# Optimization experiments

Measured on AMD Instinct MI355X. Metric: run time of the kernel, lower is better.

## Reference

```python
import jax, jax.numpy as jnp
import numpy as np

# E2M1 FP4 code table: code = sign(1b) | magnitude(3b)
FP4_VALS = jnp.array([0.0, 0.5, 1.0, 1.5, 2.0, 3.0, 4.0, 6.0,
                      -0.0, -0.5, -1.0, -1.5, -2.0, -3.0, -4.0, -6.0], dtype=jnp.float32)
ALPHA = 1.702
LIMIT = 7.0
BLOCK = 32


def dequant_mxfp4(qw, scales):
    """qw: [N, K//2] byte values (two 4-bit codes, low nibble first);
    scales: [N, K//32] E8M0 exponents. Returns fp32 [N, K]."""
    lo = qw & 0xF
    hi = (qw >> 4) & 0xF
    codes = jnp.stack([lo, hi], axis=-1).reshape(qw.shape[0], -1)  # [N, K]
    w = FP4_VALS[codes]
    s = jnp.exp2((scales - 127).astype(jnp.float32))               # [N, K//32]
    N, K = w.shape
    w = w.reshape(N, K // BLOCK, BLOCK) * s[..., None]
    return w.reshape(N, K)


def setup_inputs() -> dict:
    key = jax.random.key(0)
    ks = jax.random.split(key, 9)
    T, H, I, E, TOPK = 1024, 2880, 2880, 8, 2
    return {
        "hidden_states": jax.random.normal(ks[0], (T, H), dtype=jnp.float32),
        "routing_weights": jax.random.uniform(ks[1], (T, TOPK), dtype=jnp.float32),
        "gate_up_proj_bias": jax.random.normal(ks[2], (E, 2 * I), dtype=jnp.float32),
        "down_proj_bias": jax.random.normal(ks[3], (E, H), dtype=jnp.float32),
        "router_indices": jax.random.randint(ks[4], (T, TOPK), 0, E, dtype=jnp.int32),
        "gate_up_qweight": jax.random.randint(ks[5], (E, 2 * I, H // 2), 0, 256, dtype=jnp.int32),
        "gate_up_scales": jax.random.randint(ks[6], (E, 2 * I, H // BLOCK), 118, 130, dtype=jnp.int32),
        "down_qweight": jax.random.randint(ks[7], (E, H, I // 2), 0, 256, dtype=jnp.int32),
        "down_scales": jax.random.randint(ks[8], (E, H, I // BLOCK), 118, 130, dtype=jnp.int32),
    }


def reference(hidden_states, routing_weights, gate_up_proj_bias, down_proj_bias,
              router_indices, gate_up_qweight, gate_up_scales, down_qweight, down_scales):
    E = gate_up_qweight.shape[0]
    out = jnp.zeros_like(hidden_states)
    for e in range(E):  # small fixed expert count
        # combined routing weight per token for expert e (0 if not routed);
        # equals the index_add over all top_k hits in the original loop
        w_e = jnp.sum(jnp.where(router_indices == e, routing_weights, 0.0), axis=-1)  # [T]
        wg = dequant_mxfp4(gate_up_qweight[e], gate_up_scales[e])  # [2I, H]
        gate_up = hidden_states @ wg.T + gate_up_proj_bias[e]      # [T, 2I]
        gate = jnp.minimum(gate_up[..., 0::2], LIMIT)
        up = jnp.clip(gate_up[..., 1::2], -LIMIT, LIMIT)
        glu = gate * jax.nn.sigmoid(gate * ALPHA)
        gated = (up + 1.0) * glu                                   # [T, I]
        wd = dequant_mxfp4(down_qweight[e], down_scales[e])        # [H, I]
        o = gated @ wd.T + down_proj_bias[e]                       # [T, H]
        out = out + o * w_e[:, None]
    return out
```

## Files before the change

kernel.cpp:

```cpp
#include <hip/hip_runtime.h>
#include <hip/hip_bf16.h>

typedef unsigned int uint;
typedef unsigned short ushort;
typedef __bf16 bf16x8 __attribute__((ext_vector_type(8)));
typedef float f32x4 __attribute__((ext_vector_type(4)));
typedef unsigned short u16x2 __attribute__((ext_vector_type(2)));

#define T_TOK 1024
#define HDIM 2880
#define IDIM 2880
#define NEXP 8
#define GU 5760
#define QK1 1440
#define SG1 90
#define QK2 1440
#define SG2 90
#define MAXR 2048
#define NK 45

#define BM 384
#define BGU 192
#define BNH 64

#define LDA 72

#define LISTS_OFF 256
#define HB_OFF (1u << 17)
#define GATED_OFF_PRE 6029312u
#define GATED_OFF_RAW (1u << 17)
#define WS_NEED (GATED_OFF_PRE + (size_t)MAXR * IDIM * 2)


static __device__ __forceinline__ uint pkadd16(uint a, uint b) {
  u16x2 x = __builtin_bit_cast(u16x2, a);
  u16x2 y = __builtin_bit_cast(u16x2, b);
  u16x2 r = x + y;
  return __builtin_bit_cast(uint, r);
}

static __device__ __forceinline__ void decode8(uint P, uint sAdd2, uint out[4]) {
  uint L  = P & 0x0F0F0F0Fu;
  uint Hh = (P >> 4) & 0x0F0F0F0Fu;
  uint Lm = L & 0x07070707u,  Hm = Hh & 0x07070707u;
  uint Lsg = (L & 0x08080808u) << 4, Hsg = (Hh & 0x08080808u) << 4;
  uint hiL = __builtin_amdgcn_perm(0x40404040u, 0x3F3F3F00u, Lm) | Lsg;
  uint hiH = __builtin_amdgcn_perm(0x40404040u, 0x3F3F3F00u, Hm) | Hsg;
  uint loL = __builtin_amdgcn_perm(0xC0804000u, 0xC0800000u, Lm);
  uint loH = __builtin_amdgcn_perm(0xC0804000u, 0xC0800000u, Hm);
  uint mL  = __builtin_amdgcn_perm(0xFFFFFFFFu, 0xFFFFFF00u, Lm);
  uint mH  = __builtin_amdgcn_perm(0xFFFFFFFFu, 0xFFFFFF00u, Hm);
  uint pL01 = __builtin_amdgcn_perm(hiL, loL, 0x05010400u);
  uint pL23 = __builtin_amdgcn_perm(hiL, loL, 0x07030602u);
  uint pH01 = __builtin_amdgcn_perm(hiH, loH, 0x05010400u);
  uint pH23 = __builtin_amdgcn_perm(hiH, loH, 0x07030602u);
  uint aL01 = pkadd16(pL01, sAdd2 & __builtin_amdgcn_perm(mL, mL, 0x01010000u));
  uint aL23 = pkadd16(pL23, sAdd2 & __builtin_amdgcn_perm(mL, mL, 0x03030202u));
  uint aH01 = pkadd16(pH01, sAdd2 & __builtin_amdgcn_perm(mH, mH, 0x01010000u));
  uint aH23 = pkadd16(pH23, sAdd2 & __builtin_amdgcn_perm(mH, mH, 0x03030202u));
  out[0] = __builtin_amdgcn_perm(aH01, aL01, 0x05040100u);
  out[1] = __builtin_amdgcn_perm(aH01, aL01, 0x07060302u);
  out[2] = __builtin_amdgcn_perm(aH23, aL23, 0x05040100u);
  out[3] = __builtin_amdgcn_perm(aH23, aL23, 0x07060302u);
}

static __device__ __forceinline__ uint packbf2(float a, float b) {
  ushort ua = __builtin_bit_cast(ushort, __float2bfloat16(a));
  ushort ub = __builtin_bit_cast(ushort, __float2bfloat16(b));
  return (uint)ua | ((uint)ub << 16);
}


__global__ void build_lists_kernel(const int* __restrict__ ridx,
                                   int* __restrict__ counts,
                                   int* __restrict__ lists) {
  int r = blockIdx.x * 256 + threadIdx.x;
  if (r >= MAXR) return;
  int e = ridx[r];
  int pos = atomicAdd(&counts[e], 1);
  lists[e * MAXR + pos] = r;
}


__global__ void cvt_kernel(const float* __restrict__ in, ushort* __restrict__ out) {
  int i = (blockIdx.x * 256 + threadIdx.x) * 8;
  float4 a = *(const float4*)(in + i);
  float4 b = *(const float4*)(in + i + 4);
  uint4 o;
  o.x = packbf2(a.x, a.y); o.y = packbf2(a.z, a.w);
  o.z = packbf2(b.x, b.y); o.w = packbf2(b.z, b.w);
  *(uint4*)(out + i) = o;
}


template <bool PRE>
__global__ __launch_bounds__(512, 2)
void gemm1_kernel(const float* __restrict__ hiddenF,
                  const ushort* __restrict__ hiddenB,
                  const int* __restrict__ guq,
                  const int* __restrict__ gus,
                  const float* __restrict__ gub,
                  const int* __restrict__ counts,
                  const int* __restrict__ lists,
                  ushort* __restrict__ gated) {
  const int e = blockIdx.z;
  const int cnt = counts[e];
  const int mt = blockIdx.y;
  if (mt * BM >= cnt) return;
  const int gu0 = blockIdx.x * BGU;
  const int tid = threadIdx.x;

  extern __shared__ char smem[];
  ushort* lA = (ushort*)smem;
  ushort* lB = lA + BM * LDA;
  int* rowid = (int*)(lB + BGU * LDA);

  for (int i = tid; i < BM; i += 512) {
    int rl = mt * BM + i;
    rowid[i] = (rl < cnt) ? lists[e * MAXR + rl] : -1;
  }
  __syncthreads();

  const int srow = tid >> 3;
  const int soff = tid & 7;

  uint avalid = 0;
  const ushort* aB[6];
  const float*  aF[6];
  #pragma unroll
  for (int j = 0; j < 6; ++j) {
    int r = rowid[srow + 64 * j];
    if (r >= 0) avalid |= (1u << j);
    int tok = (r >= 0) ? (r >> 1) : 0;
    if (PRE) aB[j] = hiddenB + (size_t)tok * HDIM + soff * 8;
    else     aF[j] = hiddenF + (size_t)tok * HDIM + soff * 8;
  }
  const size_t jrow0 = (size_t)e * GU + gu0 + srow;
  const int* bq0 = guq + jrow0 * QK1 + soff * 4;
  const int* bs0 = gus + jrow0 * SG1 + (soff >> 2);

  f32x4 acc[6][6];
  #pragma unroll
  for (int m = 0; m < 6; ++m)
    #pragma unroll
    for (int n = 0; n < 6; ++n) acc[m][n] = (f32x4)0.f;

  const int ln = tid & 63;
  const int ln15 = ln & 15, kq = ln >> 4;
  const int wv = tid >> 6, wm = wv & 3, wn = wv >> 2;

  uint4 aP[6];
  int4  bP[3];
  int   sP[3];

  auto load_step = [&](int k0) {
    #pragma unroll
    for (int j = 0; j < 6; ++j) {
      if (avalid & (1u << j)) {
        if (PRE) {
          aP[j] = *(const uint4*)(aB[j] + k0);
        } else {
          float4 f0 = *(const float4*)(aF[j] + k0);
          float4 f1 = *(const float4*)(aF[j] + k0 + 4);
          aP[j].x = packbf2(f0.x, f0.y); aP[j].y = packbf2(f0.z, f0.w);
          aP[j].z = packbf2(f1.x, f1.y); aP[j].w = packbf2(f1.z, f1.w);
        }
      } else {
        aP[j].x = aP[j].y = aP[j].z = aP[j].w = 0u;
      }
    }
    #pragma unroll
    for (int j = 0; j < 3; ++j) {
      bP[j] = *(const int4*)(bq0 + (size_t)j * 64 * QK1 + (k0 >> 1));
      sP[j] = *(bs0 + (size_t)j * 64 * SG1 + (k0 >> 5));
    }
  };

  load_step(0);

  for (int ks = 0; ks < NK; ++ks) {
    #pragma unroll
    for (int j = 0; j < 6; ++j)
      *(uint4*)&lA[(srow + 64 * j) * LDA + soff * 8] = aP[j];
    #pragma unroll
    for (int j = 0; j < 3; ++j) {
      uint P = (uint)bP[j].x | ((uint)bP[j].y << 8) |
               ((uint)bP[j].z << 16) | ((uint)bP[j].w << 24);
      uint sOff = ((uint)(sP[j] - 127) << 7) & 0xFFFFu;
      uint sAdd2 = sOff | (sOff << 16);
      uint o[4];
      decode8(P, sAdd2, o);
      uint4 w; w.x = o[0]; w.y = o[1]; w.z = o[2]; w.w = o[3];
      *(uint4*)&lB[(srow + 64 * j) * LDA + soff * 8] = w;
    }
    __syncthreads();
    if (ks + 1 < NK) load_step((ks + 1) * 64);
    #pragma unroll
    for (int kf = 0; kf < 2; ++kf) {
      const int ko = kf * 32 + kq * 8;
      bf16x8 bfr[6];
      #pragma unroll
      for (int n = 0; n < 6; ++n)
        bfr[n] = *(const bf16x8*)&lB[(wn * 96 + n * 16 + ln15) * LDA + ko];
      #pragma unroll
      for (int m = 0; m < 6; ++m) {
        bf16x8 af = *(const bf16x8*)&lA[(wm * 96 + m * 16 + ln15) * LDA + ko];
        #pragma unroll
        for (int n = 0; n < 6; ++n)
          acc[m][n] = __builtin_amdgcn_mfma_f32_16x16x32_bf16(af, bfr[n], acc[m][n], 0, 0, 0);
      }
    }
    __syncthreads();
  }

  float bias[6];
  #pragma unroll
  for (int n = 0; n < 6; ++n)
    bias[n] = gub[(size_t)e * GU + gu0 + wn * 96 + n * 16 + ln15];
  #pragma unroll
  for (int m = 0; m < 6; ++m) {
    #pragma unroll
    for (int rg = 0; rg < 4; ++rg) {
      int rl = wm * 96 + m * 16 + kq * 4 + rg;
      int r = rowid[rl];
      #pragma unroll
      for (int n = 0; n < 6; ++n) {
        float x = acc[m][n][rg] + bias[n];
        float y = __shfl_xor(x, 1);
        if (r >= 0 && !(ln & 1)) {
          float g = fminf(x, 7.f);
          float u = fminf(fmaxf(y, -7.f), 7.f);
          float glu = g / (1.f + __expf(-1.702f * g));
          float val = (u + 1.f) * glu;
          int gucol = gu0 + wn * 96 + n * 16 + ln15;
          gated[(size_t)r * IDIM + (gucol >> 1)] =
              __builtin_bit_cast(ushort, __float2bfloat16(val));
        }
      }
    }
  }
}


__global__ __launch_bounds__(512, 2)
void gemm2_kernel(const ushort* __restrict__ gated,
                  const int* __restrict__ dq,
                  const int* __restrict__ dsc,
                  const float* __restrict__ dpb,
                  const float* __restrict__ routing,
                  const int* __restrict__ counts,
                  const int* __restrict__ lists,
                  float* __restrict__ outp) {
  const int e = blockIdx.z;
  const int cnt = counts[e];
  const int mt = blockIdx.y;
  if (mt * BM >= cnt) return;
  const int h0 = blockIdx.x * BNH;
  const int tid = threadIdx.x;

  extern __shared__ char smem[];
  ushort* lA = (ushort*)smem;
  ushort* lB = lA + BM * LDA;
  int* rowid = (int*)(lB + BNH * LDA);

  for (int i = tid; i < BM; i += 512) {
    int rl = mt * BM + i;
    rowid[i] = (rl < cnt) ? lists[e * MAXR + rl] : -1;
  }
  __syncthreads();

  const int srow = tid >> 3;
  const int soff = tid & 7;

  uint avalid = 0;
  const ushort* aB[6];
  #pragma unroll
  for (int j = 0; j < 6; ++j) {
    int r = rowid[srow + 64 * j];
    if (r >= 0) avalid |= (1u << j);
    int rr = (r >= 0) ? r : 0;
    aB[j] = gated + (size_t)rr * IDIM + soff * 8;
  }
  const size_t hrow = (size_t)e * HDIM + h0 + srow;
  const int* bq0 = dq + hrow * QK2 + soff * 4;
  const int* bs0 = dsc + hrow * SG2 + (soff >> 2);

  f32x4 acc[6][2];
  #pragma unroll
  for (int m = 0; m < 6; ++m) {
    acc[m][0] = (f32x4)0.f;
    acc[m][1] = (f32x4)0.f;
  }

  const int ln = tid & 63;
  const int ln15 = ln & 15, kq = ln >> 4;
  const int wv = tid >> 6, wm = wv & 3, wn = wv >> 2;

  uint4 aP[6];
  int4  bP;
  int   sP;

  auto load_step = [&](int k0) {
    #pragma unroll
    for (int j = 0; j < 6; ++j) {
      if (avalid & (1u << j)) aP[j] = *(const uint4*)(aB[j] + k0);
      else { aP[j].x = aP[j].y = aP[j].z = aP[j].w = 0u; }
    }
    bP = *(const int4*)(bq0 + (k0 >> 1));
    sP = *(bs0 + (k0 >> 5));
  };

  load_step(0);

  for (int ks = 0; ks < NK; ++ks) {
    #pragma unroll
    for (int j = 0; j < 6; ++j)
      *(uint4*)&lA[(srow + 64 * j) * LDA + soff * 8] = aP[j];
    {
      uint P = (uint)bP.x | ((uint)bP.y << 8) | ((uint)bP.z << 16) | ((uint)bP.w << 24);
      uint sOff = ((uint)(sP - 127) << 7) & 0xFFFFu;
      uint sAdd2 = sOff | (sOff << 16);
      uint o[4];
      decode8(P, sAdd2, o);
      uint4 w; w.x = o[0]; w.y = o[1]; w.z = o[2]; w.w = o[3];
      *(uint4*)&lB[srow * LDA + soff * 8] = w;
    }
    __syncthreads();
    if (ks + 1 < NK) load_step((ks + 1) * 64);
    #pragma unroll
    for (int kf = 0; kf < 2; ++kf) {
      const int ko = kf * 32 + kq * 8;
      bf16x8 bfr[2];
      #pragma unroll
      for (int n = 0; n < 2; ++n)
        bfr[n] = *(const bf16x8*)&lB[(wn * 32 + n * 16 + ln15) * LDA + ko];
      #pragma unroll
      for (int m = 0; m < 6; ++m) {
        bf16x8 af = *(const bf16x8*)&lA[(wm * 96 + m * 16 + ln15) * LDA + ko];
        #pragma unroll
        for (int n = 0; n < 2; ++n)
          acc[m][n] = __builtin_amdgcn_mfma_f32_16x16x32_bf16(af, bfr[n], acc[m][n], 0, 0, 0);
      }
    }
    __syncthreads();
  }

  float bias[2];
  #pragma unroll
  for (int n = 0; n < 2; ++n)
    bias[n] = dpb[(size_t)e * HDIM + h0 + wn * 32 + n * 16 + ln15];
  #pragma unroll
  for (int m = 0; m < 6; ++m) {
    #pragma unroll
    for (int rg = 0; rg < 4; ++rg) {
      int rl = wm * 96 + m * 16 + kq * 4 + rg;
      int r = rowid[rl];
      if (r < 0) continue;
      float wgt = routing[r];
      #pragma unroll
      for (int n = 0; n < 2; ++n) {
        int hcol = h0 + wn * 32 + n * 16 + ln15;
        atomicAdd(outp + (size_t)(r >> 1) * HDIM + hcol,
                  wgt * (acc[m][n][rg] + bias[n]));
      }
    }
  }
}


extern "C" void kernel_launch(void* const* d_in, const int* in_sizes, int n_in,
                              void* d_out, int out_size, void* d_ws, size_t ws_size,
                              hipStream_t stream) {
  const float* hidden  = (const float*)d_in[0];
  const float* routing = (const float*)d_in[1];
  const float* gub     = (const float*)d_in[2];
  const float* dpb     = (const float*)d_in[3];
  const int*   ridx    = (const int*)d_in[4];
  const int*   guq     = (const int*)d_in[5];
  const int*   gus     = (const int*)d_in[6];
  const int*   dq      = (const int*)d_in[7];
  const int*   dsc     = (const int*)d_in[8];
  float* outp = (float*)d_out;

  char* ws = (char*)d_ws;
  int* counts = (int*)ws;
  int* lists  = (int*)(ws + LISTS_OFF);
  const bool pre = (ws_size >= WS_NEED);
  ushort* hb    = (ushort*)(ws + HB_OFF);
  ushort* gated = (ushort*)(ws + (pre ? GATED_OFF_PRE : GATED_OFF_RAW));

  const int LDS1 = (BM * LDA + BGU * LDA) * 2 + BM * 4;
  const int LDS2 = (BM * LDA + BNH * LDA) * 2 + BM * 4;
  if (pre)
    hipFuncSetAttribute((const void*)gemm1_kernel<true>,
                        hipFuncAttributeMaxDynamicSharedMemorySize, LDS1);
  else
    hipFuncSetAttribute((const void*)gemm1_kernel<false>,
                        hipFuncAttributeMaxDynamicSharedMemorySize, LDS1);
  hipFuncSetAttribute((const void*)gemm2_kernel,
                      hipFuncAttributeMaxDynamicSharedMemorySize, LDS2);

  hipMemsetAsync(counts, 0, 256, stream);
  hipMemsetAsync(d_out, 0, (size_t)out_size * sizeof(float), stream);

  build_lists_kernel<<<MAXR / 256, 256, 0, stream>>>(ridx, counts, lists);
  if (pre)
    cvt_kernel<<<(T_TOK * HDIM / 8) / 256, 256, 0, stream>>>(hidden, hb);

  dim3 grid1(GU / BGU, (MAXR + BM - 1) / BM, NEXP);
  if (pre)
    gemm1_kernel<true><<<grid1, 512, LDS1, stream>>>(hidden, hb, guq, gus, gub,
                                                     counts, lists, gated);
  else
    gemm1_kernel<false><<<grid1, 512, LDS1, stream>>>(hidden, hb, guq, gus, gub,
                                                      counts, lists, gated);

  dim3 grid2(HDIM / BNH, (MAXR + BM - 1) / BM, NEXP);
  gemm2_kernel<<<grid2, 512, LDS2, stream>>>(gated, dq, dsc, dpb, routing,
                                             counts, lists, outp);
}
```

Baseline: 262.6 us.

## Retile expert GEMMs with async global-to-LDS loads and XOR-swizzled shared memory

Both expert GEMMs are restructured into 256-thread blocks with smaller N tiles (64 for gate/up, 32 for down) and a 320-row M tile, with experts interleaved in the x grid dimension. Activation tiles are now loaded straight into LDS with global_load_lds, using a zeroed dummy row for padding, in place of register staging. The padded LDS layout is replaced by an XOR swizzle, and s_setprio is raised around the MFMA section. This is meant to raise occupancy and cut register-staging and bank-conflict costs. In exchange it drops the previous register prefetch of the next step and decodes the weights more often because the N tiles are smaller.

```diff
diff --git a/kernel.cpp b/kernel.cpp
--- a/kernel.cpp
+++ b/kernel.cpp
@@ -18,19 +18,16 @@
 #define SG2 90
 #define MAXR 2048
 #define NK 45
-
-#define BM 384
-#define BGU 192
-#define BNH 64
-
-#define LDA 72
-
-#define LISTS_OFF 256
-#define HB_OFF (1u << 17)
+#define BM 320
+
+#define ZROW_OFF 65536u
+#define HB_OFF 131072u
 #define GATED_OFF_PRE 6029312u
-#define GATED_OFF_RAW (1u << 17)
 #define WS_NEED (GATED_OFF_PRE + (size_t)MAXR * IDIM * 2)
 
+static __device__ __forceinline__ int ls(int row, int c) {
+  return (row << 6) + (((c ^ row) & 7) << 3);
+}
 
 static __device__ __forceinline__ uint pkadd16(uint a, uint b) {
   u16x2 x = __builtin_bit_cast(u16x2, a);
@@ -94,137 +91,145 @@
 
 
 template <bool PRE>
-__global__ __launch_bounds__(512, 2)
-void gemm1_kernel(const float* __restrict__ hiddenF,
-                  const ushort* __restrict__ hiddenB,
+__global__ __launch_bounds__(256, 3)
+void gemm1_kernel(const char* __restrict__ wsb,
+                  const float* __restrict__ hiddenF,
                   const int* __restrict__ guq,
                   const int* __restrict__ gus,
                   const float* __restrict__ gub,
                   const int* __restrict__ counts,
                   const int* __restrict__ lists,
                   ushort* __restrict__ gated) {
-  const int e = blockIdx.z;
+  const int e  = blockIdx.x & 7;
+  const int xt = blockIdx.x >> 3;
   const int cnt = counts[e];
   const int mt = blockIdx.y;
   if (mt * BM >= cnt) return;
-  const int gu0 = blockIdx.x * BGU;
+  const int gu0 = xt * 64;
   const int tid = threadIdx.x;
 
-  extern __shared__ char smem[];
-  ushort* lA = (ushort*)smem;
-  ushort* lB = lA + BM * LDA;
-  int* rowid = (int*)(lB + BGU * LDA);
-
-  for (int i = tid; i < BM; i += 512) {
+  __shared__ ushort lA[BM * 64];
+  __shared__ ushort lB[64 * 64];
+  __shared__ int rowid[BM];
+
+  for (int i = tid; i < BM; i += 256) {
     int rl = mt * BM + i;
     rowid[i] = (rl < cnt) ? lists[e * MAXR + rl] : -1;
   }
   __syncthreads();
 
-  const int srow = tid >> 3;
-  const int soff = tid & 7;
-
+  const int ln = tid & 63, wv = tid >> 6;
+  const int ln15 = ln & 15, kq = ln >> 4;
+
+  uint aoff[10];
   uint avalid = 0;
-  const ushort* aB[6];
-  const float*  aF[6];
-  #pragma unroll
-  for (int j = 0; j < 6; ++j) {
-    int r = rowid[srow + 64 * j];
-    if (r >= 0) avalid |= (1u << j);
-    int tok = (r >= 0) ? (r >> 1) : 0;
-    if (PRE) aB[j] = hiddenB + (size_t)tok * HDIM + soff * 8;
-    else     aF[j] = hiddenF + (size_t)tok * HDIM + soff * 8;
-  }
-  const size_t jrow0 = (size_t)e * GU + gu0 + srow;
-  const int* bq0 = guq + jrow0 * QK1 + soff * 4;
-  const int* bs0 = gus + jrow0 * SG1 + (soff >> 2);
-
-  f32x4 acc[6][6];
-  #pragma unroll
-  for (int m = 0; m < 6; ++m)
-    #pragma unroll
-    for (int n = 0; n < 6; ++n) acc[m][n] = (f32x4)0.f;
-
-  const int ln = tid & 63;
-  const int ln15 = ln & 15, kq = ln >> 4;
-  const int wv = tid >> 6, wm = wv & 3, wn = wv >> 2;
-
-  uint4 aP[6];
-  int4  bP[3];
-  int   sP[3];
-
-  auto load_step = [&](int k0) {
-    #pragma unroll
-    for (int j = 0; j < 6; ++j) {
-      if (avalid & (1u << j)) {
-        if (PRE) {
-          aP[j] = *(const uint4*)(aB[j] + k0);
-        } else {
-          float4 f0 = *(const float4*)(aF[j] + k0);
-          float4 f1 = *(const float4*)(aF[j] + k0 + 4);
-          aP[j].x = packbf2(f0.x, f0.y); aP[j].y = packbf2(f0.z, f0.w);
-          aP[j].z = packbf2(f1.x, f1.y); aP[j].w = packbf2(f1.z, f1.w);
-        }
-      } else {
-        aP[j].x = aP[j].y = aP[j].z = aP[j].w = 0u;
-      }
-    }
-    #pragma unroll
-    for (int j = 0; j < 3; ++j) {
-      bP[j] = *(const int4*)(bq0 + (size_t)j * 64 * QK1 + (k0 >> 1));
-      sP[j] = *(bs0 + (size_t)j * 64 * SG1 + (k0 >> 5));
-    }
-  };
-
-  load_step(0);
+  if (PRE) {
+    #pragma unroll
+    for (int j = 0; j < 10; ++j) {
+      int slot = wv * 640 + j * 64 + ln;
+      int row  = slot >> 3;
+      int corig = (slot ^ row) & 7;
+      int r = rowid[row];
+      aoff[j] = (r >= 0) ? (HB_OFF + (uint)(r >> 1) * (HDIM * 2) + corig * 16)
+                         : (ZROW_OFF + corig * 16);
+    }
+  } else {
+    #pragma unroll
+    for (int j = 0; j < 10; ++j) {
+      int row = (tid >> 3) + 32 * j;
+      int r = rowid[row];
+      if (r >= 0) avalid |= 1u << j;
+      uint tok = (r >= 0) ? (uint)(r >> 1) : 0u;
+      aoff[j] = tok * (HDIM * 4) + (uint)(tid & 7) * 32;
+    }
+  }
+
+  const int brow = tid >> 2, c2 = tid & 3;
+  const uint grow = (uint)(e * GU + gu0 + brow);
+  const uint boff0 = grow * (QK1 * 4) + (uint)c2 * 32;
+  const uint soff0 = grow * (SG1 * 4) + (uint)(c2 >> 1) * 4;
+
+  f32x4 acc[5][4];
+  #pragma unroll
+  for (int m = 0; m < 5; ++m)
+    #pragma unroll
+    for (int n = 0; n < 4; ++n) acc[m][n] = (f32x4)0.f;
+
+  const char* gq = (const char*)guq;
+  const char* gs = (const char*)gus;
 
   for (int ks = 0; ks < NK; ++ks) {
-    #pragma unroll
-    for (int j = 0; j < 6; ++j)
-      *(uint4*)&lA[(srow + 64 * j) * LDA + soff * 8] = aP[j];
-    #pragma unroll
-    for (int j = 0; j < 3; ++j) {
-      uint P = (uint)bP[j].x | ((uint)bP[j].y << 8) |
-               ((uint)bP[j].z << 16) | ((uint)bP[j].w << 24);
-      uint sOff = ((uint)(sP[j] - 127) << 7) & 0xFFFFu;
+    int4 bv0 = *(const int4*)(gq + boff0 + (uint)ks * 128);
+    int4 bv1 = *(const int4*)(gq + boff0 + (uint)ks * 128 + 16);
+    int  sv  = *(const int*)(gs + soff0 + (uint)ks * 8);
+    if (PRE) {
+      #pragma unroll
+      for (int j = 0; j < 10; ++j) {
+        __builtin_amdgcn_global_load_lds(
+            (const __attribute__((address_space(1))) void*)(wsb + aoff[j] + (uint)ks * 128),
+            (__attribute__((address_space(3))) void*)((char*)lA + (wv * 640 + j * 64) * 16),
+            16, 0, 0);
+      }
+    } else {
+      #pragma unroll
+      for (int j = 0; j < 10; ++j) {
+        int row = (tid >> 3) + 32 * j;
+        uint4 o;
+        if (avalid & (1u << j)) {
+          const float4* f = (const float4*)((const char*)hiddenF + aoff[j] + (size_t)ks * 256);
+          float4 f0 = f[0], f1 = f[1];
+          o.x = packbf2(f0.x, f0.y); o.y = packbf2(f0.z, f0.w);
+          o.z = packbf2(f1.x, f1.y); o.w = packbf2(f1.z, f1.w);
+        } else { o.x = o.y = o.z = o.w = 0u; }
+        *(uint4*)&lA[ls(row, tid & 7)] = o;
+      }
+    }
+    {
+      uint P0 = (uint)bv0.x | ((uint)bv0.y << 8) | ((uint)bv0.z << 16) | ((uint)bv0.w << 24);
+      uint P1 = (uint)bv1.x | ((uint)bv1.y << 8) | ((uint)bv1.z << 16) | ((uint)bv1.w << 24);
+      uint sOff = ((uint)(sv - 127) << 7) & 0xFFFFu;
       uint sAdd2 = sOff | (sOff << 16);
-      uint o[4];
-      decode8(P, sAdd2, o);
-      uint4 w; w.x = o[0]; w.y = o[1]; w.z = o[2]; w.w = o[3];
-      *(uint4*)&lB[(srow + 64 * j) * LDA + soff * 8] = w;
+      uint o0[4], o1[4];
+      decode8(P0, sAdd2, o0);
+      decode8(P1, sAdd2, o1);
+      uint4 w0; w0.x = o0[0]; w0.y = o0[1]; w0.z = o0[2]; w0.w = o0[3];
+      uint4 w1; w1.x = o1[0]; w1.y = o1[1]; w1.z = o1[2]; w1.w = o1[3];
+      *(uint4*)&lB[ls(brow, 2 * c2)]     = w0;
+      *(uint4*)&lB[ls(brow, 2 * c2 + 1)] = w1;
     }
     __syncthreads();
-    if (ks + 1 < NK) load_step((ks + 1) * 64);
+    __builtin_amdgcn_s_setprio(1);
     #pragma unroll
     for (int kf = 0; kf < 2; ++kf) {
-      const int ko = kf * 32 + kq * 8;
-      bf16x8 bfr[6];
-      #pragma unroll
-      for (int n = 0; n < 6; ++n)
-        bfr[n] = *(const bf16x8*)&lB[(wn * 96 + n * 16 + ln15) * LDA + ko];
-      #pragma unroll
-      for (int m = 0; m < 6; ++m) {
-        bf16x8 af = *(const bf16x8*)&lA[(wm * 96 + m * 16 + ln15) * LDA + ko];
+      const int cc = 4 * kf + kq;
+      bf16x8 bfr[4];
+      #pragma unroll
+      for (int n = 0; n < 4; ++n)
+        bfr[n] = *(const bf16x8*)&lB[ls(n * 16 + ln15, cc)];
+      #pragma unroll
+      for (int m = 0; m < 5; ++m) {
+        bf16x8 af = *(const bf16x8*)&lA[ls(wv * 80 + m * 16 + ln15, cc)];
         #pragma unroll
-        for (int n = 0; n < 6; ++n)
+        for (int n = 0; n < 4; ++n)
           acc[m][n] = __builtin_amdgcn_mfma_f32_16x16x32_bf16(af, bfr[n], acc[m][n], 0, 0, 0);
       }
     }
+    __builtin_amdgcn_s_setprio(0);
     __syncthreads();
   }
 
-  float bias[6];
-  #pragma unroll
-  for (int n = 0; n < 6; ++n)
-    bias[n] = gub[(size_t)e * GU + gu0 + wn * 96 + n * 16 + ln15];
-  #pragma unroll
-  for (int m = 0; m < 6; ++m) {
+  float bias[4];
+  #pragma unroll
+  for (int n = 0; n < 4; ++n)
+    bias[n] = gub[(size_t)e * GU + gu0 + n * 16 + ln15];
+  #pragma unroll
+  for (int m = 0; m < 5; ++m) {
     #pragma unroll
     for (int rg = 0; rg < 4; ++rg) {
-      int rl = wm * 96 + m * 16 + kq * 4 + rg;
-      int r = rowid[rl];
-      #pragma unroll
-      for (int n = 0; n < 6; ++n) {
+      int row = wv * 80 + m * 16 + kq * 4 + rg;
+      int r = rowid[row];
+      #pragma unroll
+      for (int n = 0; n < 4; ++n) {
         float x = acc[m][n][rg] + bias[n];
         float y = __shfl_xor(x, 1);
         if (r >= 0 && !(ln & 1)) {
@@ -232,7 +237,7 @@
           float u = fminf(fmaxf(y, -7.f), 7.f);
           float glu = g / (1.f + __expf(-1.702f * g));
           float val = (u + 1.f) * glu;
-          int gucol = gu0 + wn * 96 + n * 16 + ln15;
+          int gucol = gu0 + n * 16 + ln15;
           gated[(size_t)r * IDIM + (gucol >> 1)] =
               __builtin_bit_cast(ushort, __float2bfloat16(val));
         }
@@ -242,8 +247,8 @@
 }
 
 
-__global__ __launch_bounds__(512, 2)
-void gemm2_kernel(const ushort* __restrict__ gated,
+__global__ __launch_bounds__(256, 3)
+void gemm2_kernel(const char* __restrict__ wsb, uint gatedOff,
                   const int* __restrict__ dq,
                   const int* __restrict__ dsc,
                   const float* __restrict__ dpb,
@@ -251,115 +256,113 @@
                   const int* __restrict__ counts,
                   const int* __restrict__ lists,
                   float* __restrict__ outp) {
-  const int e = blockIdx.z;
+  const int e  = blockIdx.x & 7;
+  const int ht = blockIdx.x >> 3;
   const int cnt = counts[e];
   const int mt = blockIdx.y;
   if (mt * BM >= cnt) return;
-  const int h0 = blockIdx.x * BNH;
+  const int h0 = ht * 32;
   const int tid = threadIdx.x;
 
-  extern __shared__ char smem[];
-  ushort* lA = (ushort*)smem;
-  ushort* lB = lA + BM * LDA;
-  int* rowid = (int*)(lB + BNH * LDA);
-
-  for (int i = tid; i < BM; i += 512) {
+  __shared__ ushort lA[BM * 64];
+  __shared__ ushort lB[32 * 64];
+  __shared__ int rowid[BM];
+
+  for (int i = tid; i < BM; i += 256) {
     int rl = mt * BM + i;
     rowid[i] = (rl < cnt) ? lists[e * MAXR + rl] : -1;
   }
   __syncthreads();
 
-  const int srow = tid >> 3;
-  const int soff = tid & 7;
-
-  uint avalid = 0;
-  const ushort* aB[6];
-  #pragma unroll
-  for (int j = 0; j < 6; ++j) {
-    int r = rowid[srow + 64 * j];
-    if (r >= 0) avalid |= (1u << j);
-    int rr = (r >= 0) ? r : 0;
-    aB[j] = gated + (size_t)rr * IDIM + soff * 8;
-  }
-  const size_t hrow = (size_t)e * HDIM + h0 + srow;
-  const int* bq0 = dq + hrow * QK2 + soff * 4;
-  const int* bs0 = dsc + hrow * SG2 + (soff >> 2);
-
-  f32x4 acc[6][2];
-  #pragma unroll
-  for (int m = 0; m < 6; ++m) {
-    acc[m][0] = (f32x4)0.f;
-    acc[m][1] = (f32x4)0.f;
-  }
-
-  const int ln = tid & 63;
+  const int ln = tid & 63, wv = tid >> 6;
   const int ln15 = ln & 15, kq = ln >> 4;
-  const int wv = tid >> 6, wm = wv & 3, wn = wv >> 2;
-
-  uint4 aP[6];
-  int4  bP;
-  int   sP;
-
-  auto load_step = [&](int k0) {
-    #pragma unroll
-    for (int j = 0; j < 6; ++j) {
-      if (avalid & (1u << j)) aP[j] = *(const uint4*)(aB[j] + k0);
-      else { aP[j].x = aP[j].y = aP[j].z = aP[j].w = 0u; }
-    }
-    bP = *(const int4*)(bq0 + (k0 >> 1));
-    sP = *(bs0 + (k0 >> 5));
-  };
-
-  load_step(0);
+
+  uint aoff[10];
+  #pragma unroll
+  for (int j = 0; j < 10; ++j) {
+    int slot = wv * 640 + j * 64 + ln;
+    int row  = slot >> 3;
+    int corig = (slot ^ row) & 7;
+    int r = rowid[row];
+    aoff[j] = (r >= 0) ? (gatedOff + (uint)r * (IDIM * 2) + corig * 16)
+                       : (ZROW_OFF + corig * 16);
+  }
+  const int brow = tid >> 2, c2 = tid & 3;
+  const bool bact = (brow < 32);
+  const uint hrow = (uint)(e * HDIM + h0 + (brow & 31));
+  const uint boff0 = hrow * (QK2 * 4) + (uint)c2 * 32;
+  const uint soff0 = hrow * (SG2 * 4) + (uint)(c2 >> 1) * 4;
+
+  f32x4 acc[5][2];
+  #pragma unroll
+  for (int m = 0; m < 5; ++m) { acc[m][0] = (f32x4)0.f; acc[m][1] = (f32x4)0.f; }
+
+  const char* gq = (const char*)dq;
+  const char* gs = (const char*)dsc;
 
   for (int ks = 0; ks < NK; ++ks) {
-    #pragma unroll
-    for (int j = 0; j < 6; ++j)
-      *(uint4*)&lA[(srow + 64 * j) * LDA + soff * 8] = aP[j];
-    {
-      uint P = (uint)bP.x | ((uint)bP.y << 8) | ((uint)bP.z << 16) | ((uint)bP.w << 24);
-      uint sOff = ((uint)(sP - 127) << 7) & 0xFFFFu;
+    int4 bv0, bv1; int sv = 0;
+    if (bact) {
+      bv0 = *(const int4*)(gq + boff0 + (uint)ks * 128);
+      bv1 = *(const int4*)(gq + boff0 + (uint)ks * 128 + 16);
+      sv  = *(const int*)(gs + soff0 + (uint)ks * 8);
+    }
+    #pragma unroll
+    for (int j = 0; j < 10; ++j) {
+      __builtin_amdgcn_global_load_lds(
+          (const __attribute__((address_space(1))) void*)(wsb + aoff[j] + (uint)ks * 128),
+          (__attribute__((address_space(3))) void*)((char*)lA + (wv * 640 + j * 64) * 16),
+          16, 0, 0);
+    }
+    if (bact) {
+      uint P0 = (uint)bv0.x | ((uint)bv0.y << 8) | ((uint)bv0.z << 16) | ((uint)bv0.w << 24);
+      uint P1 = (uint)bv1.x | ((uint)bv1.y << 8) | ((uint)bv1.z << 16) | ((uint)bv1.w << 24);
+      uint sOff = ((uint)(sv - 127) << 7) & 0xFFFFu;
       uint sAdd2 = sOff | (sOff << 16);
-      uint o[4];
-      decode8(P, sAdd2, o);
-      uint4 w; w.x = o[0]; w.y = o[1]; w.z = o[2]; w.w = o[3];
-      *(uint4*)&lB[srow * LDA + soff * 8] = w;
+      uint o0[4], o1[4];
+      decode8(P0, sAdd2, o0);
+      decode8(P1, sAdd2, o1);
+      uint4 w0; w0.x = o0[0]; w0.y = o0[1]; w0.z = o0[2]; w0.w = o0[3];
+      uint4 w1; w1.x = o1[0]; w1.y = o1[1]; w1.z = o1[2]; w1.w = o1[3];
+      *(uint4*)&lB[ls(brow & 31, 2 * c2)]     = w0;
+      *(uint4*)&lB[ls(brow & 31, 2 * c2 + 1)] = w1;
     }
     __syncthreads();
-    if (ks + 1 < NK) load_step((ks + 1) * 64);
+    __builtin_amdgcn_s_setprio(1);
     #pragma unroll
     for (int kf = 0; kf < 2; ++kf) {
-      const int ko = kf * 32 + kq * 8;
+      const int cc = 4 * kf + kq;
       bf16x8 bfr[2];
       #pragma unroll
       for (int n = 0; n < 2; ++n)
-        bfr[n] = *(const bf16x8*)&lB[(wn * 32 + n * 16 + ln15) * LDA + ko];
-      #pragma unroll
-      for (int m = 0; m < 6; ++m) {
-        bf16x8 af = *(const bf16x8*)&lA[(wm * 96 + m * 16 + ln15) * LDA + ko];
+        bfr[n] = *(const bf16x8*)&lB[ls(n * 16 + ln15, cc)];
+      #pragma unroll
+      for (int m = 0; m < 5; ++m) {
+        bf16x8 af = *(const bf16x8*)&lA[ls(wv * 80 + m * 16 + ln15, cc)];
         #pragma unroll
         for (int n = 0; n < 2; ++n)
           acc[m][n] = __builtin_amdgcn_mfma_f32_16x16x32_bf16(af, bfr[n], acc[m][n], 0, 0, 0);
       }
     }
+    __builtin_amdgcn_s_setprio(0);
     __syncthreads();
   }
 
   float bias[2];
   #pragma unroll
   for (int n = 0; n < 2; ++n)
-    bias[n] = dpb[(size_t)e * HDIM + h0 + wn * 32 + n * 16 + ln15];
-  #pragma unroll
-  for (int m = 0; m < 6; ++m) {
+    bias[n] = dpb[(size_t)e * HDIM + h0 + n * 16 + ln15];
+  #pragma unroll
+  for (int m = 0; m < 5; ++m) {
     #pragma unroll
     for (int rg = 0; rg < 4; ++rg) {
-      int rl = wm * 96 + m * 16 + kq * 4 + rg;
-      int r = rowid[rl];
+      int row = wv * 80 + m * 16 + kq * 4 + rg;
+      int r = rowid[row];
       if (r < 0) continue;
       float wgt = routing[r];
       #pragma unroll
       for (int n = 0; n < 2; ++n) {
-        int hcol = h0 + wn * 32 + n * 16 + ln15;
+        int hcol = h0 + n * 16 + ln15;
         atomicAdd(outp + (size_t)(r >> 1) * HDIM + hcol,
                   wgt * (acc[m][n][rg] + bias[n]));
       }
@@ -384,38 +387,29 @@
 
   char* ws = (char*)d_ws;
   int* counts = (int*)ws;
-  int* lists  = (int*)(ws + LISTS_OFF);
+  int* lists  = (int*)(ws + 256);
   const bool pre = (ws_size >= WS_NEED);
+  const uint gatedOff = pre ? GATED_OFF_PRE : HB_OFF;
   ushort* hb    = (ushort*)(ws + HB_OFF);
-  ushort* gated = (ushort*)(ws + (pre ? GATED_OFF_PRE : GATED_OFF_RAW));
-
-  const int LDS1 = (BM * LDA + BGU * LDA) * 2 + BM * 4;
-  const int LDS2 = (BM * LDA + BNH * LDA) * 2 + BM * 4;
-  if (pre)
-    hipFuncSetAttribute((const void*)gemm1_kernel<true>,
-                        hipFuncAttributeMaxDynamicSharedMemorySize, LDS1);
-  else
-    hipFuncSetAttribute((const void*)gemm1_kernel<false>,
-                        hipFuncAttributeMaxDynamicSharedMemorySize, LDS1);
-  hipFuncSetAttribute((const void*)gemm2_kernel,
-                      hipFuncAttributeMaxDynamicSharedMemorySize, LDS2);
+  ushort* gated = (ushort*)(ws + gatedOff);
 
   hipMemsetAsync(counts, 0, 256, stream);
+  hipMemsetAsync(ws + ZROW_OFF, 0, 5760, stream);
   hipMemsetAsync(d_out, 0, (size_t)out_size * sizeof(float), stream);
 
   build_lists_kernel<<<MAXR / 256, 256, 0, stream>>>(ridx, counts, lists);
   if (pre)
     cvt_kernel<<<(T_TOK * HDIM / 8) / 256, 256, 0, stream>>>(hidden, hb);
 
-  dim3 grid1(GU / BGU, (MAXR + BM - 1) / BM, NEXP);
+  dim3 grid1((GU / 64) * NEXP, (MAXR + BM - 1) / BM);
   if (pre)
-    gemm1_kernel<true><<<grid1, 512, LDS1, stream>>>(hidden, hb, guq, gus, gub,
-                                                     counts, lists, gated);
+    gemm1_kernel<true><<<grid1, 256, 0, stream>>>(ws, hidden, guq, gus, gub,
+                                                  counts, lists, gated);
   else
-    gemm1_kernel<false><<<grid1, 512, LDS1, stream>>>(hidden, hb, guq, gus, gub,
-                                                      counts, lists, gated);
-
-  dim3 grid2(HDIM / BNH, (MAXR + BM - 1) / BM, NEXP);
-  gemm2_kernel<<<grid2, 512, LDS2, stream>>>(gated, dq, dsc, dpb, routing,
-                                             counts, lists, outp);
-}
+    gemm1_kernel<false><<<grid1, 256, 0, stream>>>(ws, hidden, guq, gus, gub,
+                                                   counts, lists, gated);
+
+  dim3 grid2((HDIM / 32) * NEXP, (MAXR + BM - 1) / BM);
+  gemm2_kernel<<<grid2, 256, 0, stream>>>(ws, gatedOff, dq, dsc, dpb, routing,
+                                          counts, lists, outp);
+}
```

Result: slower. 289.7 us (+10.3%).
